# Kernel tuning notes

Hardware: AMD Instinct MI355X
Metric: run time of the kernel (lower is better)

The kernel has to match this reference:

```python
import jax, jax.numpy as jnp
import numpy as np

B, S, H = 64, 2048, 512
VOCAB = 40000


def setup_inputs() -> dict:
    key = jax.random.key(0)
    k1, k2, k3, k4, k5 = jax.random.split(key, 5)
    token_ids = jax.random.randint(k1, (B, S), 0, VOCAB, dtype=jnp.int64) if jax.config.jax_enable_x64 else jax.random.randint(k1, (B, S), 0, VOCAB, dtype=jnp.int32)
    std = 0.02
    pos_table = jax.random.normal(k2, (S, H), dtype=jnp.float32) * std
    nest_table = jax.random.normal(k3, (16, H), dtype=jnp.float32) * std
    seg_table = jax.random.normal(k4, (8, H), dtype=jnp.float32) * std
    W = jax.random.normal(k5, (3 * H, H), dtype=jnp.float32) * (1.0 / np.sqrt(3 * H))
    return {"token_ids": token_ids, "pos_table": pos_table, "nest_table": nest_table, "seg_table": seg_table, "W": W}


def _syntax_info(token_ids):
    # Parallel replacement for the serial per-token loop.
    t = token_ids
    opens = (t == 40) | (t == 123) | (t == 91)
    closes = (t == 41) | (t == 125) | (t == 93)
    delta = opens.astype(jnp.int32) - closes.astype(jnp.int32)
    s = jnp.cumsum(delta, axis=1)  # unclamped walk
    # Lindley recursion level_i = max(0, level_{i-1} + d_i)
    #   == s_i - min(0, min_{j<=i} s_j)
    run_min = jax.lax.cummin(s, axis=1)
    nesting = jnp.clip(s - jnp.minimum(run_min, 0), 0, 15)
    segments = jnp.cumsum((t > 39990).astype(jnp.int32), axis=1) % 8
    return nesting, segments


def reference(token_ids, pos_table, nest_table, seg_table, W):
    b, s = token_ids.shape
    positions = jnp.arange(s)
    pos_emb = jnp.broadcast_to(pos_table[positions][None], (b, s, pos_table.shape[-1]))
    nesting, segments = _syntax_info(token_ids)
    nest_emb = nest_table[nesting]      # [B,S,H]
    seg_emb = seg_table[segments]       # [B,S,H]
    combined = jnp.concatenate([pos_emb, nest_emb, seg_emb], axis=-1)  # [B,S,3H]
    return jnp.einsum('bsk,kh->bsh', combined, W)
```

## Files before the change

### kernel.cpp

```cpp
#include <hip/hip_runtime.h>
#include <cstdint>

#define BB 64
#define SS 2048

__global__ __launch_bounds__(256) void prep_kernel(
    const int* __restrict__ tok, const float* __restrict__ pos,
    const float* __restrict__ nest, const float* __restrict__ seg,
    const float* __restrict__ W,
    int* __restrict__ idx, float* __restrict__ P, float* __restrict__ NG) {
    const int blk = blockIdx.x;
    const int tid = threadIdx.x;

    if (blk < 256) {
        __shared__ float As[16][68];
        __shared__ float Bs[16][64];
        const int bm = (blk >> 3) << 6;
        const int bn = (blk & 7) << 6;
        const int am = tid >> 2, ak = (tid & 3) << 2;
        const int bk = tid >> 4, bn2 = (tid & 15) << 2;
        const int tn = tid & 15, tm = tid >> 4;

        const float* Ap = pos + (size_t)(bm + am) * 512 + ak;
        const float* Bp = W + (size_t)bk * 512 + bn + bn2;
        float4 aR = *(const float4*)Ap;
        float4 bR = *(const float4*)Bp;

        float acc[4][4];
#pragma unroll
        for (int i = 0; i < 4; ++i)
#pragma unroll
            for (int j = 0; j < 4; ++j) acc[i][j] = 0.0f;

        for (int k0 = 0; k0 < 512; k0 += 16) {
            __syncthreads();
            As[ak + 0][am] = aR.x; As[ak + 1][am] = aR.y;
            As[ak + 2][am] = aR.z; As[ak + 3][am] = aR.w;
            *(float4*)&Bs[bk][bn2] = bR;
            __syncthreads();
            if (k0 + 16 < 512) {
                aR = *(const float4*)(Ap + k0 + 16);
                bR = *(const float4*)(Bp + (size_t)(k0 + 16) * 512);
            }
#pragma unroll
            for (int kk = 0; kk < 16; ++kk) {
                float4 a = *(const float4*)&As[kk][tm << 2];
                float4 b = *(const float4*)&Bs[kk][tn << 2];
                float av[4] = {a.x, a.y, a.z, a.w};
                float bv[4] = {b.x, b.y, b.z, b.w};
#pragma unroll
                for (int i = 0; i < 4; ++i)
#pragma unroll
                    for (int j = 0; j < 4; ++j) acc[i][j] += av[i] * bv[j];
            }
        }
#pragma unroll
        for (int i = 0; i < 4; ++i) {
            float4 o = make_float4(acc[i][0], acc[i][1], acc[i][2], acc[i][3]);
            *(float4*)(P + (size_t)(bm + (tm << 2) + i) * 512 + bn + (tn << 2)) = o;
        }
    } else if (blk < 304) {
        const int b2 = blk - 256;
        const int row = b2 >> 1;
        const int col = ((b2 & 1) << 8) + tid;
        const float* Ta = (row < 16) ? (nest + (size_t)row * 512)
                                     : (seg + (size_t)(row - 16) * 512);
        const float* Wx = W + ((row < 16) ? (size_t)512 * 512 : (size_t)1024 * 512);
        float s = 0.0f;
#pragma unroll 8
        for (int k = 0; k < 512; ++k) s += Ta[k] * Wx[(size_t)k * 512 + col];
        NG[(size_t)row * 512 + col] = s;
    } else {
        __shared__ int sS[256], sM[256], sG[256];
        const int b = blk - 304;
        const int* t = tok + (size_t)b * SS;
        int4 w0 = reinterpret_cast<const int4*>(t)[tid * 2 + 0];
        int4 w1 = reinterpret_cast<const int4*>(t)[tid * 2 + 1];
        int tk[8] = {w0.x, w0.y, w0.z, w0.w, w1.x, w1.y, w1.z, w1.w};

        int ls[8], lmin[8], lseg[8];
        int s = 0, m = 2147483647, sg = 0;
#pragma unroll
        for (int j = 0; j < 8; ++j) {
            int v = tk[j];
            int open_ = (v == 40) | (v == 123) | (v == 91);
            int close_ = (v == 41) | (v == 125) | (v == 93);
            s += open_ - close_;
            m = min(m, s);
            sg += (v > 39990) ? 1 : 0;
            ls[j] = s; lmin[j] = m; lseg[j] = sg;
        }
        sS[tid] = s; sM[tid] = m; sG[tid] = sg;
        __syncthreads();
        for (int off = 1; off < 256; off <<= 1) {
            int aS = 0, aM = 2147483647, aG = 0;
            bool has = (tid >= off);
            if (has) { aS = sS[tid - off]; aM = sM[tid - off]; aG = sG[tid - off]; }
            __syncthreads();
            if (has) {
                sM[tid] = min(aM, aS + sM[tid]);
                sS[tid] = aS + sS[tid];
                sG[tid] = aG + sG[tid];
            }
            __syncthreads();
        }
        int pS = 0, pM = 2147483647, pG = 0;
        if (tid > 0) { pS = sS[tid - 1]; pM = sM[tid - 1]; pG = sG[tid - 1]; }

        int res[8];
#pragma unroll
        for (int j = 0; j < 8; ++j) {
            int gs = pS + ls[j];
            int rm = min(pM, pS + lmin[j]);
            int nst = gs - min(rm, 0);
            nst = max(0, min(15, nst));
            int sgm = (pG + lseg[j]) & 7;
            res[j] = nst * 8 + sgm;
        }
        int4* op = reinterpret_cast<int4*>(idx + (size_t)b * SS + tid * 8);
        op[0] = make_int4(res[0], res[1], res[2], res[3]);
        op[1] = make_int4(res[4], res[5], res[6], res[7]);
    }
}

__global__ __launch_bounds__(256) void out_kernel(const float4* __restrict__ P,
                                                  const float4* __restrict__ NG,
                                                  const int* __restrict__ idx,
                                                  float4* __restrict__ out) {
    const int s = blockIdx.x >> 3;
    const int bg = blockIdx.x & 7;
    const int tx = threadIdx.x & 127;
    const int tz = threadIdx.x >> 7;

    const float4 p = P[(size_t)s * 128 + tx];
#pragma unroll
    for (int i = 0; i < 4; ++i) {
        const int b = (bg << 3) + (i << 1) + tz;
        const size_t r = (size_t)b * SS + s;
        const int id = idx[r];
        const float4 nv = NG[(size_t)(id >> 3) * 128 + tx];
        const float4 gv = NG[(size_t)(16 + (id & 7)) * 128 + tx];
        float4 o;
        o.x = p.x + nv.x + gv.x;
        o.y = p.y + nv.y + gv.y;
        o.z = p.z + nv.z + gv.z;
        o.w = p.w + nv.w + gv.w;
        out[r * 128 + tx] = o;
    }
}

extern "C" void kernel_launch(void* const* d_in, const int* in_sizes, int n_in,
                              void* d_out, int out_size, void* d_ws, size_t ws_size,
                              hipStream_t stream) {
    const int* tok = (const int*)d_in[0];
    const float* pos = (const float*)d_in[1];
    const float* nest = (const float*)d_in[2];
    const float* seg = (const float*)d_in[3];
    const float* W = (const float*)d_in[4];
    float* out = (float*)d_out;

    char* ws = (char*)d_ws;
    int* idx = (int*)ws;
    float* P = (float*)(ws + (512 << 10));
    float* NG = (float*)(ws + (512 << 10) + (4 << 20));

    prep_kernel<<<368, 256, 0, stream>>>(tok, pos, nest, seg, W, idx, P, NG);
    out_kernel<<<SS * 8, 256, 0, stream>>>(
        (const float4*)P, (const float4*)NG, idx, (float4*)out);
}
```

Before: 312.3 us.

## Process all batches per position in one block with staged indices and nontemporal stores

The output kernel now launches one block per sequence position instead of eight. Each block stages all 64 batch indices in shared memory, loads the position row once, and loops over the 64 batch rows. Stores use nontemporal hints to keep the large output stream from polluting cache, and block-to-position mapping is permuted. The launch has fewer blocks, each doing more serial work, which may reduce parallelism and latency hiding.

```diff
diff --git a/kernel.cpp b/kernel.cpp
--- a/kernel.cpp
+++ b/kernel.cpp
@@ -3,6 +3,8 @@
 
 #define BB 64
 #define SS 2048
+
+typedef float f32x4 __attribute__((ext_vector_type(4)));
 
 __global__ __launch_bounds__(256) void prep_kernel(
     const int* __restrict__ tok, const float* __restrict__ pos,
@@ -123,29 +125,28 @@
     }
 }
 
-__global__ __launch_bounds__(256) void out_kernel(const float4* __restrict__ P,
-                                                  const float4* __restrict__ NG,
+__global__ __launch_bounds__(256) void out_kernel(const f32x4* __restrict__ P,
+                                                  const f32x4* __restrict__ NG,
                                                   const int* __restrict__ idx,
-                                                  float4* __restrict__ out) {
-    const int s = blockIdx.x >> 3;
-    const int bg = blockIdx.x & 7;
+                                                  f32x4* __restrict__ out) {
+    __shared__ int sIdx[64];
+    const int bid = blockIdx.x;
+    const int s = ((bid & 7) << 8) + (bid >> 3);
     const int tx = threadIdx.x & 127;
     const int tz = threadIdx.x >> 7;
 
-    const float4 p = P[(size_t)s * 128 + tx];
-#pragma unroll
-    for (int i = 0; i < 4; ++i) {
-        const int b = (bg << 3) + (i << 1) + tz;
-        const size_t r = (size_t)b * SS + s;
-        const int id = idx[r];
-        const float4 nv = NG[(size_t)(id >> 3) * 128 + tx];
-        const float4 gv = NG[(size_t)(16 + (id & 7)) * 128 + tx];
-        float4 o;
-        o.x = p.x + nv.x + gv.x;
-        o.y = p.y + nv.y + gv.y;
-        o.z = p.z + nv.z + gv.z;
-        o.w = p.w + nv.w + gv.w;
-        out[r * 128 + tx] = o;
+    if (threadIdx.x < 64) sIdx[threadIdx.x] = idx[(size_t)threadIdx.x * SS + s];
+    const f32x4 p = P[(size_t)s * 128 + tx];
+    __syncthreads();
+
+#pragma unroll 4
+    for (int i = 0; i < 32; ++i) {
+        const int b = (i << 1) + tz;
+        const int id = sIdx[b];
+        const f32x4 nv = NG[(size_t)(id >> 3) * 128 + tx];
+        const f32x4 gv = NG[(size_t)(16 + (id & 7)) * 128 + tx];
+        f32x4 o = (p + nv) + gv;
+        __builtin_nontemporal_store(o, &out[((size_t)b * SS + s) * 128 + tx]);
     }
 }
 
@@ -165,6 +166,6 @@
     float* NG = (float*)(ws + (512 << 10) + (4 << 20));
 
     prep_kernel<<<368, 256, 0, stream>>>(tok, pos, nest, seg, W, idx, P, NG);
-    out_kernel<<<SS * 8, 256, 0, stream>>>(
-        (const float4*)P, (const float4*)NG, idx, (float4*)out);
+    out_kernel<<<2048, 256, 0, stream>>>(
+        (const f32x4*)P, (const f32x4*)NG, idx, (f32x4*)out);
 }
```

Result: no change. 315.5 us (+1.0%).
